# Optimization experiments

Measured on AMD Instinct MI355X. Metric: run time of the kernel, lower is better.

Reference implementation:

```python
import jax, jax.numpy as jnp
import numpy as np

B, S, D = 128, 50, 128
NUM_NODE = 40000
SAMPLE = 12
HOP = 2
ALPHA = 0.2  # leaky-relu slope (opt.alpha)


def _leaky(x, slope=ALPHA):
    return jnp.where(x >= 0, x, slope * x)


def setup_inputs() -> dict:
    key = jax.random.key(0)
    ks = jax.random.split(key, 12)
    stdv = 1.0 / float(np.sqrt(D))
    inputs = jax.random.randint(ks[0], (B, S), 0, NUM_NODE)
    adj = jax.random.randint(ks[1], (B, S, S), 0, 5)
    mask_item = jax.random.randint(ks[2], (B, S), 0, 2).at[:, 0].set(1)
    item = jax.random.randint(ks[3], (B, S), 0, NUM_NODE)
    adj_all = jax.random.randint(ks[4], (NUM_NODE, SAMPLE), 0, NUM_NODE)
    num_weight = jax.random.uniform(ks[5], (NUM_NODE, SAMPLE), dtype=jnp.float32)
    embedding = jax.random.uniform(ks[6], (NUM_NODE, D), minval=-stdv, maxval=stdv, dtype=jnp.float32)
    a_local = jax.random.uniform(ks[7], (4, D), minval=-stdv, maxval=stdv, dtype=jnp.float32)
    agg_w1 = jax.random.uniform(ks[8], (HOP, D + 1, D), minval=-stdv, maxval=stdv, dtype=jnp.float32)
    agg_w2 = jax.random.uniform(ks[9], (HOP, D, 1), minval=-stdv, maxval=stdv, dtype=jnp.float32)
    agg_w3 = jax.random.uniform(ks[10], (HOP, 2 * D, D), minval=-stdv, maxval=stdv, dtype=jnp.float32)
    return dict(inputs=inputs, adj=adj, mask_item=mask_item, item=item,
                adj_all=adj_all, num_weight=num_weight, embedding=embedding,
                a_local=a_local, agg_w1=agg_w1, agg_w2=agg_w2, agg_w3=agg_w3)


def _local_agg(h, adj, a_local):
    # e_k[b,i,j] = leakyrelu(sum_d h[b,i,d]*h[b,j,d]*a_k[d]); never materialize [B,N,N,D]
    e = _leaky(jnp.einsum('bid,bjd,kd->kbij', h, h, a_local))  # [4,B,S,S]
    alpha = jnp.full(e.shape[1:], -9e15, dtype=h.dtype)
    for k in range(4):
        alpha = jnp.where(adj == k + 1, e[k], alpha)
    alpha = jax.nn.softmax(alpha, axis=-1)
    return alpha @ h


def _global_agg(w1, w2, w3, self_v, neigh_v, neigh_w, extra):
    # self_v [B,L,D]; neigh_v [B,L,SAMPLE,D]; neigh_w [B,L,SAMPLE]; extra [B,L,D]
    feat = jnp.concatenate([extra[:, :, None, :] * neigh_v, neigh_w[..., None]], axis=-1)  # [B,L,SAMPLE,D+1]
    a = _leaky(feat @ w1, 0.2)                              # [B,L,SAMPLE,D]
    a = jax.nn.softmax((a @ w2)[..., 0], axis=-1)[..., None]  # [B,L,SAMPLE,1]
    neigh = jnp.sum(a * neigh_v, axis=-2)                   # [B,L,D]
    out = jnp.concatenate([self_v, neigh], axis=-1) @ w3    # [B,L,D]
    return jax.nn.relu(out)


def _forward(inputs, adj, mask_item, item, adj_all, num_weight, embedding,
             a_local, agg_w1, agg_w2, agg_w3):
    h = embedding[inputs]                          # [B,S,D]
    h_local = _local_agg(h, adj, a_local)
    # multi-hop neighbor sampling (index_select into adj_all / num)
    item_neighbors = [inputs]
    weight_neighbors = []
    support = S
    for _ in range(HOP):
        last = item_neighbors[-1].reshape(-1)
        support *= SAMPLE
        item_neighbors.append(adj_all[last].reshape(B, support))
        weight_neighbors.append(num_weight[last].reshape(B, support))
    entity = [embedding[idx] for idx in item_neighbors]
    mask_f = mask_item.astype(h.dtype)
    item_emb = embedding[item] * mask_f[..., None]
    session = (jnp.sum(item_emb, 1) / jnp.sum(mask_f, -1, keepdims=True))[:, None, :]  # [B,1,D]
    for n_hop in range(HOP):
        nxt = []
        for hop in range(HOP - n_hop):
            self_v = entity[hop]
            L = self_v.shape[1]
            neigh_v = entity[hop + 1].reshape(B, L, SAMPLE, D)
            neigh_w = weight_neighbors[hop].reshape(B, L, SAMPLE)
            extra = jnp.broadcast_to(session, (B, L, D))
            nxt.append(_global_agg(agg_w1[n_hop], agg_w2[n_hop], agg_w3[n_hop],
                                   self_v, neigh_v, neigh_w, extra))
        entity = nxt
    h_global = entity[0].reshape(B, S, D)
    # dropout_local / dropout_global are identity in eval mode
    return h_local + h_global


def reference(inputs, adj, mask_item, item, adj_all, num_weight, embedding,
              a_local, agg_w1, agg_w2, agg_w3):
    return _forward(inputs, adj, mask_item, item, adj_all, num_weight, embedding,
                    a_local, agg_w1, agg_w2, agg_w3)
```

## Files before the change

kernel.cpp:

```cpp
#include <hip/hip_runtime.h>
#include <math.h>

#define BATCH 128
#define S 50
#define D 128
#define SAMPLE 12

typedef __attribute__((ext_vector_type(8))) short short8v;
typedef __attribute__((ext_vector_type(4))) float f32x4;
typedef unsigned short u16;

__device__ __forceinline__ float leakyf(float x) { return x >= 0.f ? x : 0.2f * x; }
__device__ __forceinline__ u16 f2bf(float f) {
    union { float f; unsigned u; } v; v.f = f;
    unsigned u = v.u;
    return (u16)((u + 0x7FFFu + ((u >> 16) & 1u)) >> 16);
}
__device__ __forceinline__ float bf2f(u16 h) {
    union { float f; unsigned u; } v; v.u = ((unsigned)h) << 16; return v.f;
}

__global__ __launch_bounds__(256) void setup1_kernel(
    const int* __restrict__ item, const int* __restrict__ mask,
    const int* __restrict__ inputs, const int* __restrict__ adj_all,
    const float* __restrict__ num_weight, const float* __restrict__ emb,
    float* __restrict__ session, int* __restrict__ n1, float* __restrict__ nw0)
{
    const int bx = blockIdx.x, t = threadIdx.x;
    if (bx < BATCH) {
        if (t < 128) {
            float num = 0.f, den = 0.f;
            for (int s = 0; s < S; ++s) {
                float m = (float)mask[bx * S + s];
                num += m * emb[item[bx * S + s] * D + t];
                den += m;
            }
            session[bx * D + t] = num / den;
        }
    } else {
        int idx = (bx - BATCH) * 256 + t;
        if (idx < BATCH * 600) {
            int b = idx / 600, j = idx % 600;
            int node = inputs[b * S + j / SAMPLE];
            n1[idx]  = adj_all[node * SAMPLE + j % SAMPLE];
            nw0[idx] = num_weight[node * SAMPLE + j % SAMPLE];
        }
    }
}

__global__ __launch_bounds__(256) void prep2_kernel(
    const float* __restrict__ emb, const float* __restrict__ w1,
    const float* __restrict__ w3, const float* __restrict__ session,
    const int* __restrict__ adj_all, const float* __restrict__ num_weight,
    const int* __restrict__ n1,
    u16* __restrict__ emb_bf, u16* __restrict__ sw1, u16* __restrict__ w3t,
    int* __restrict__ n2p, int* __restrict__ n1p, float* __restrict__ nw1)
{
    const int bx = blockIdx.x, t = threadIdx.x;
    if (bx < 2500) {
        int idx = bx * 256 + t;
        const float4* src = reinterpret_cast<const float4*>(emb) + (size_t)idx * 2;
        float4 a = src[0], c = src[1];
        u16 o[8] = {f2bf(a.x), f2bf(a.y), f2bf(a.z), f2bf(a.w),
                    f2bf(c.x), f2bf(c.y), f2bf(c.z), f2bf(c.w)};
        *reinterpret_cast<uint4*>(emb_bf + (size_t)idx * 8) = *reinterpret_cast<uint4*>(o);
    } else if (bx < 2756) {
        int id = bx - 2500, hop = id >> 7, b = id & 127;
        const float* w1s = w1 + hop * 129 * 128;
        const float* se = session + b * 128;
        int n = t >> 1, kh = (t & 1) * 64;
        u16* dst = sw1 + (((size_t)(hop * 128 + b) * 128 + n) * 128) + kh;
        for (int kq = 0; kq < 64; kq += 8) {
            u16 o[8];
            #pragma unroll
            for (int e = 0; e < 8; ++e) { int k = kh + kq + e; o[e] = f2bf(w1s[k * 128 + n] * se[k]); }
            *reinterpret_cast<uint4*>(dst + kq) = *reinterpret_cast<uint4*>(o);
        }
    } else if (bx < 2788) {
        int j = (bx - 2756) * 256 + t;
        int hop = j >> 12, r = j & 4095, n = r >> 5, k0 = (r & 31) * 8;
        const float* w3s = w3 + hop * 256 * 128;
        u16 o[8];
        #pragma unroll
        for (int e = 0; e < 8; ++e) o[e] = f2bf(w3s[(k0 + e) * 128 + n]);
        *reinterpret_cast<uint4*>(w3t + ((size_t)hop * 128 + n) * 256 + k0) = *reinterpret_cast<uint4*>(o);
    } else if (bx < 6388) {
        int idx = (bx - 2788) * 256 + t;
        if (idx < BATCH * 7200) {
            int b = idx / 7200, r = idx % 7200;
            int lblk = r / 96, q = r % 96;
            int i = q >> 4, c = q & 15;
            int gm = lblk * 96 + (c >> 2) * 24 + i * 4 + (c & 3);
            int node = n1[b * 600 + gm / SAMPLE];
            int s = gm % SAMPLE;
            n2p[idx] = adj_all[node * SAMPLE + s] << 8;
            nw1[b * 7200 + gm] = num_weight[node * SAMPLE + s];
        }
    } else {
        int idx = (bx - 6388) * 256 + t;
        if (idx < BATCH * 672) {
            int b = idx / 672, r = idx % 672;
            int lblk = r / 96, q = r % 96;
            int i = q >> 4, c = q & 15;
            int gm = lblk * 96 + (c >> 2) * 24 + i * 4 + (c & 3);
            int jc = (gm < 600) ? gm : 0;
            n1p[idx] = n1[b * 600 + jc] << 8;
        }
    }
}

template <int PATH>
__global__ __launch_bounds__(256, 4) void main_kernel(
    const int* __restrict__ inputs, const int* __restrict__ adj,
    const u16* __restrict__ emb_bf, const float* __restrict__ a_local,
    const int* __restrict__ n1, const int* __restrict__ n2p,
    const int* __restrict__ n1p,
    const float* __restrict__ nw0, const float* __restrict__ nw1,
    const u16* __restrict__ sw1, const float* __restrict__ w1,
    const float* __restrict__ w2, const u16* __restrict__ w3t,
    const u16* __restrict__ in0, const u16* __restrict__ in1,
    u16* __restrict__ o0, u16* __restrict__ o1, float* __restrict__ outf)
{
    __shared__ __align__(16) char smem[30976];
    const int b = blockIdx.y;
    const int t = threadIdx.x;
    const int bx = blockIdx.x;

    if (PATH == 0 && bx == 0) {
        u16*   ht    = (u16*)smem;
        float* alpha = (float*)(smem + 13312);
        u16*   alb   = (u16*)(smem + 23520);

        for (int idx = t; idx < S * D; idx += 256) {
            int i = idx >> 7, d = idx & 127;
            ht[d * 52 + i] = emb_bf[(size_t)inputs[b * S + i] * D + d];
        }
        for (int idx = t; idx < 512; idx += 256) alb[idx] = f2bf(a_local[idx]);
        __syncthreads();

        for (int p = t; p < S * S; p += 256) {
            int i = p / S, j = p % S;
            int a = adj[b * S * S + p];
            float v = -9e15f;
            if (a >= 1 && a <= 4) {
                const u16* ak = alb + (a - 1) * D;
                float dot = 0.f;
                #pragma unroll 4
                for (int d = 0; d < D; ++d)
                    dot += bf2f(ht[d * 52 + i]) * bf2f(ht[d * 52 + j]) * bf2f(ak[d]);
                v = leakyf(dot);
            }
            alpha[i * 51 + j] = v;
        }
        __syncthreads();

        if (t < S) {
            float m = -INFINITY;
            for (int j = 0; j < S; ++j) m = fmaxf(m, alpha[t * 51 + j]);
            float ssum = 0.f;
            for (int j = 0; j < S; ++j) { float e = __expf(alpha[t * 51 + j] - m); alpha[t * 51 + j] = e; ssum += e; }
            float inv = 1.f / ssum;
            for (int j = 0; j < S; ++j) alpha[t * 51 + j] *= inv;
        }
        __syncthreads();

        for (int idx = t; idx < S * D; idx += 256) {
            int i = idx >> 7, d = idx & 127;
            float acc = 0.f;
            #pragma unroll 5
            for (int j = 0; j < S; ++j) acc += alpha[i * 51 + j] * bf2f(ht[d * 52 + j]);
            outf[(size_t)b * S * D + idx] = acc;
        }
        return;
    }

    int mode, lblk, L, Lm, hop;
    const u16 *nsrc, *ssrc;
    const int* ptab; const float* nwTab;
    u16* outb;
    if (PATH == 2)    { mode = 2; lblk = bx;     L = 50;  Lm = 600;  hop = 1; nsrc = in1;    ssrc = in0;    ptab = nullptr;                   nwTab = nw0; outb = nullptr; }
    else if (bx >= 8) { mode = 1; lblk = bx - 8; L = 600; Lm = 7200; hop = 0; nsrc = emb_bf; ssrc = emb_bf; ptab = n2p + (b * 75 + lblk) * 96; nwTab = nw1; outb = o1; }
    else              { mode = 0; lblk = bx - 1; L = 50;  Lm = 600;  hop = 0; nsrc = emb_bf; ssrc = emb_bf; ptab = n1p + (b * 7 + lblk) * 96;  nwTab = nw0; outb = o0; }
    const int l0 = lblk * 8;

    u16*   nvL     = (u16*)smem;
    u16*   selfL   = (u16*)(smem + 24576);
    float* score_w = (float*)(smem + 28672);
    float* nwgtL   = (float*)(smem + 30208);
    float* alphL   = (float*)(smem + 30592);

    const u16*   sw1b   = sw1 + (size_t)(hop * 128 + b) * 16384;
    const float* w1last = w1 + hop * 129 * 128 + 128 * 128;
    const float* w2h    = w2 + hop * 128;
    const u16*   w3th   = w3t + hop * 32768;

    const int lane = t & 63, wv = t >> 6, cn = lane & 15, cg = lane >> 4;
    const int nc0 = (2 * wv) * 16 + cn, nc1 = (2 * wv + 1) * 16 + cn;
    const int c = t & 15;
    const int chunk = t >> 4;

    #pragma unroll
    for (int i = 0; i < 6; ++i) {
        int off;
        if (PATH == 2) {
            int gm = l0 * 12 + (c >> 2) * 24 + i * 4 + (c & 3);
            if (gm > 599) gm = 599;
            off = (b * 600 + gm) << 8;
        } else {
            off = ptab[i * 16 + c];
        }
        uint4 v = *reinterpret_cast<const uint4*>((const char*)nsrc + (unsigned)off + chunk * 16);
        *reinterpret_cast<uint4*>(nvL + (i * 256 + t) * 8) = v;
    }
    {
        int l = 2 * (c >> 2) + ((c >> 1) & 1);
        int lg = l0 + l; if (lg >= L) lg = 0;
        int srow;
        if (PATH == 2)      srow = b * 50 + lg;
        else if (mode == 1) srow = n1[b * 600 + lg];
        else                srow = inputs[b * S + lg];
        uint4 v = *reinterpret_cast<const uint4*>(ssrc + (size_t)srow * 128 + chunk * 8);
        *reinterpret_cast<uint4*>(selfL + t * 8) = v;
    }
    if (t < 96) {
        int gm = l0 * 12 + t;
        nwgtL[t] = (gm < Lm) ? nwTab[b * Lm + gm] : 0.f;
    }
    __syncthreads();

    f32x4 acc[6][2];
    #pragma unroll
    for (int mt = 0; mt < 6; ++mt) {
        acc[mt][0] = (f32x4){0.f, 0.f, 0.f, 0.f};
        acc[mt][1] = (f32x4){0.f, 0.f, 0.f, 0.f};
    }
    #pragma unroll
    for (int kk = 0; kk < 4; ++kk) {
        int kb = kk * 32 + cg * 8;
        short8v b0 = *reinterpret_cast<const short8v*>(sw1b + nc0 * 128 + kb);
        short8v b1 = *reinterpret_cast<const short8v*>(sw1b + nc1 * 128 + kb);
        #pragma unroll
        for (int mt = 0; mt < 6; ++mt) {
            short8v a = *reinterpret_cast<const short8v*>(nvL + ((mt * 4 + kk) * 64 + lane) * 8);
            acc[mt][0] = __builtin_amdgcn_mfma_f32_16x16x32_bf16(a, b0, acc[mt][0], 0, 0, 0);
            acc[mt][1] = __builtin_amdgcn_mfma_f32_16x16x32_bf16(a, b1, acc[mt][1], 0, 0, 0);
        }
    }
    {
        float w2v0 = w2h[nc0], w2v1 = w2h[nc1];
        float w1l0 = w1last[nc0], w1l1 = w1last[nc1];
        #pragma unroll
        for (int mt = 0; mt < 6; ++mt) {
            #pragma unroll
            for (int r = 0; r < 4; ++r) {
                int m = cg * 24 + mt * 4 + r;
                float nw = nwgtL[m];
                float v = leakyf(acc[mt][0][r] + nw * w1l0) * w2v0 +
                          leakyf(acc[mt][1][r] + nw * w1l1) * w2v1;
                v += __shfl_xor(v, 1); v += __shfl_xor(v, 2);
                v += __shfl_xor(v, 4); v += __shfl_xor(v, 8);
                if (cn == 0) score_w[m * 4 + wv] = v;
            }
        }
    }
    __syncthreads();

    {
        float alph[24];
        const f32x4* sw4 = reinterpret_cast<const f32x4*>(score_w);
        float mx0 = -1e30f, mx1 = -1e30f;
        #pragma unroll
        for (int q = 0; q < 24; ++q) {
            f32x4 s4 = sw4[cg * 24 + q];
            float s = (s4[0] + s4[1]) + (s4[2] + s4[3]);
            alph[q] = s;
            if (q < 12) mx0 = fmaxf(mx0, s); else mx1 = fmaxf(mx1, s);
        }
        float sm0 = 0.f, sm1 = 0.f;
        #pragma unroll
        for (int q = 0; q < 12; ++q) { alph[q] = __expf(alph[q] - mx0); sm0 += alph[q]; }
        #pragma unroll
        for (int q = 12; q < 24; ++q) { alph[q] = __expf(alph[q] - mx1); sm1 += alph[q]; }
        float i0 = 1.f / sm0, i1 = 1.f / sm1;
        if (cn == 0) {
            #pragma unroll
            for (int q = 0; q < 12; ++q)  alphL[cg * 24 + q] = alph[q] * i0;
            #pragma unroll
            for (int q = 12; q < 24; ++q) alphL[cg * 24 + q] = alph[q] * i1;
        }
    }

    volatile const float* alphV = alphL;
    #pragma unroll
    for (int j = 0; j < 2; ++j) {
        int nc = (2 * wv + j) * 16 + cn;
        f32x4 Y[6]; f32x4 Ys = (f32x4){0.f, 0.f, 0.f, 0.f};
        #pragma unroll
        for (int mt = 0; mt < 6; ++mt) Y[mt] = (f32x4){0.f, 0.f, 0.f, 0.f};
        #pragma unroll
        for (int kk = 0; kk < 4; ++kk) {
            int kb = kk * 32 + cg * 8;
            short8v bw = *reinterpret_cast<const short8v*>(w3th + nc * 256 + 128 + kb);
            short8v bs = *reinterpret_cast<const short8v*>(w3th + nc * 256 + kb);
            short8v aS = *reinterpret_cast<const short8v*>(selfL + (kk * 64 + lane) * 8);
            Ys = __builtin_amdgcn_mfma_f32_16x16x32_bf16(aS, bs, Ys, 0, 0, 0);
            #pragma unroll
            for (int mt = 0; mt < 6; ++mt) {
                short8v a = *reinterpret_cast<const short8v*>(nvL + ((mt * 4 + kk) * 64 + lane) * 8);
                Y[mt] = __builtin_amdgcn_mfma_f32_16x16x32_bf16(a, bw, Y[mt], 0, 0, 0);
            }
        }
        float P0 = 0.f, P1 = 0.f;
        #pragma unroll
        for (int q = 0; q < 12; ++q) P0 += alphV[cg * 24 + q] * Y[q >> 2][q & 3];
        #pragma unroll
        for (int q = 12; q < 24; ++q) P1 += alphV[cg * 24 + q] * Y[q >> 2][q & 3];
        float v0 = fmaxf(P0 + Ys[0], 0.f);
        float v1 = fmaxf(P1 + Ys[2], 0.f);
        int lg0 = l0 + cg * 2, lg1 = lg0 + 1;
        if (PATH == 2) {
            if (lg0 < L) { float* p = outf + ((size_t)b * 50 + lg0) * 128 + nc; *p += v0; }
            if (lg1 < L) { float* p = outf + ((size_t)b * 50 + lg1) * 128 + nc; *p += v1; }
        } else {
            if (lg0 < L) outb[((size_t)b * L + lg0) * 128 + nc] = f2bf(v0);
            if (lg1 < L) outb[((size_t)b * L + lg1) * 128 + nc] = f2bf(v1);
        }
    }
}

extern "C" void kernel_launch(void* const* d_in, const int* in_sizes, int n_in,
                              void* d_out, int out_size, void* d_ws, size_t ws_size,
                              hipStream_t stream)
{
    const int*   inputs     = (const int*)d_in[0];
    const int*   adj        = (const int*)d_in[1];
    const int*   mask_item  = (const int*)d_in[2];
    const int*   item       = (const int*)d_in[3];
    const int*   adj_all    = (const int*)d_in[4];
    const float* num_weight = (const float*)d_in[5];
    const float* embedding  = (const float*)d_in[6];
    const float* a_local    = (const float*)d_in[7];
    const float* agg_w1     = (const float*)d_in[8];
    const float* agg_w2     = (const float*)d_in[9];
    const float* agg_w3     = (const float*)d_in[10];
    float* out = (float*)d_out;

    char* w = (char*)d_ws;
    float* ws_session = (float*)(w);
    int*   ws_n1      = (int*)(w + 65536);
    float* ws_nw0     = (float*)(w + 372736);
    float* ws_nw1     = (float*)(w + 679936);
    int*   ws_n2p     = (int*)(w + 4366336);
    int*   ws_n1p     = (int*)(w + 8052736);
    u16*   ws_emb     = (u16*)(w + 8396800);
    u16*   ws_sw1     = (u16*)(w + 18636800);
    u16*   ws_w3t     = (u16*)(w + 27025408);
    u16*   ws_out0    = (u16*)(w + 27156480);
    u16*   ws_out1    = (u16*)(w + 28794880);

    setup1_kernel<<<dim3(BATCH + 300), 256, 0, stream>>>(
        item, mask_item, inputs, adj_all, num_weight, embedding,
        ws_session, ws_n1, ws_nw0);
    prep2_kernel<<<dim3(6724), 256, 0, stream>>>(
        embedding, agg_w1, agg_w3, ws_session, adj_all, num_weight, ws_n1,
        ws_emb, ws_sw1, ws_w3t, ws_n2p, ws_n1p, ws_nw1);

    main_kernel<0><<<dim3(83, BATCH), 256, 0, stream>>>(
        inputs, adj, ws_emb, a_local, ws_n1, ws_n2p, ws_n1p, ws_nw0, ws_nw1,
        ws_sw1, agg_w1, agg_w2, ws_w3t,
        nullptr, nullptr, ws_out0, ws_out1, out);

    main_kernel<2><<<dim3(7, BATCH), 256, 0, stream>>>(
        inputs, adj, ws_emb, a_local, ws_n1, ws_n2p, ws_n1p, ws_nw0, ws_nw1,
        ws_sw1, agg_w1, agg_w2, ws_w3t,
        ws_out0, ws_out1, nullptr, nullptr, out);
}
```

Before: 348.6 us.

## Aggregate neighbors before W3 GEMM and swizzle LDS tile layout

Reorders the math so the softmax-weighted sum of neighbor embeddings is formed first (in LDS, converted to bf16), then a single concatenated [self|neigh] x W3 MFMA GEMM runs over K=256. This replaces the earlier scheme of multiplying every neighbor sample by W3 and reducing afterwards, which cuts the second-stage MFMA work by roughly the sample count. The neighbor tile is also XOR-swizzled in LDS so the aggregation reads avoid bank conflicts. The cost is an extra LDS pass, a barrier and a little more shared memory, and the aggregated vector is rounded to bf16 before the GEMM.

```diff
diff --git a/kernel.cpp b/kernel.cpp
--- a/kernel.cpp
+++ b/kernel.cpp
@@ -109,6 +109,8 @@
     }
 }
 
+__device__ __forceinline__ int swz(int cg, int kk) { return ((kk & 1) << 2) | cg; }
+
 template <int PATH>
 __global__ __launch_bounds__(256, 4) void main_kernel(
     const int* __restrict__ inputs, const int* __restrict__ adj,
@@ -121,7 +123,7 @@
     const u16* __restrict__ in0, const u16* __restrict__ in1,
     u16* __restrict__ o0, u16* __restrict__ o1, float* __restrict__ outf)
 {
-    __shared__ __align__(16) char smem[30976];
+    __shared__ __align__(16) char smem[35072];
     const int b = blockIdx.y;
     const int t = threadIdx.x;
     const int bx = blockIdx.x;
@@ -184,10 +186,10 @@
     const int l0 = lblk * 8;
 
     u16*   nvL     = (u16*)smem;
-    u16*   selfL   = (u16*)(smem + 24576);
-    float* score_w = (float*)(smem + 28672);
-    float* nwgtL   = (float*)(smem + 30208);
-    float* alphL   = (float*)(smem + 30592);
+    u16*   A2      = (u16*)(smem + 24576);
+    float* score_w = (float*)(smem + 32768);
+    float* nwgtL   = (float*)(smem + 34304);
+    float* alphL   = (float*)(smem + 34688);
 
     const u16*   sw1b   = sw1 + (size_t)(hop * 128 + b) * 16384;
     const float* w1last = w1 + hop * 129 * 128 + 128 * 128;
@@ -196,31 +198,41 @@
 
     const int lane = t & 63, wv = t >> 6, cn = lane & 15, cg = lane >> 4;
     const int nc0 = (2 * wv) * 16 + cn, nc1 = (2 * wv + 1) * 16 + cn;
-    const int c = t & 15;
+    const int cS = t & 15;
     const int chunk = t >> 4;
 
-    #pragma unroll
-    for (int i = 0; i < 6; ++i) {
-        int off;
-        if (PATH == 2) {
-            int gm = l0 * 12 + (c >> 2) * 24 + i * 4 + (c & 3);
-            if (gm > 599) gm = 599;
-            off = (b * 600 + gm) << 8;
-        } else {
-            off = ptab[i * 16 + c];
-        }
-        uint4 v = *reinterpret_cast<const uint4*>((const char*)nsrc + (unsigned)off + chunk * 16);
-        *reinterpret_cast<uint4*>(nvL + (i * 256 + t) * 8) = v;
-    }
     {
-        int l = 2 * (c >> 2) + ((c >> 1) & 1);
-        int lg = l0 + l; if (lg >= L) lg = 0;
-        int srow;
-        if (PATH == 2)      srow = b * 50 + lg;
-        else if (mode == 1) srow = n1[b * 600 + lg];
-        else                srow = inputs[b * S + lg];
-        uint4 v = *reinterpret_cast<const uint4*>(ssrc + (size_t)srow * 128 + chunk * 8);
-        *reinterpret_cast<uint4*>(selfL + t * 8) = v;
+        int kkS = t >> 6, cgS = (t >> 4) & 3;
+        int cn2 = cS ^ swz(cgS, kkS);
+        #pragma unroll
+        for (int i = 0; i < 6; ++i) {
+            int off;
+            if (PATH == 2) {
+                int gm = l0 * 12 + (cn2 >> 2) * 24 + i * 4 + (cn2 & 3);
+                if (gm > 599) gm = 599;
+                off = (b * 600 + gm) << 8;
+            } else {
+                off = ptab[i * 16 + cn2];
+            }
+            uint4 v = *reinterpret_cast<const uint4*>((const char*)nsrc + (unsigned)off + chunk * 16);
+            *reinterpret_cast<uint4*>(nvL + (i * 256 + t) * 8) = v;
+        }
+    }
+    {
+        uint4 v = make_uint4(0, 0, 0, 0);
+        if (cS < 8) {
+            int lg = l0 + cS; if (lg >= L) lg = 0;
+            int srow;
+            if (PATH == 2)      srow = b * 50 + lg;
+            else if (mode == 1) srow = n1[b * 600 + lg];
+            else                srow = inputs[b * S + lg];
+            v = *reinterpret_cast<const uint4*>(ssrc + (size_t)srow * 128 + chunk * 8);
+        }
+        *reinterpret_cast<uint4*>(A2 + t * 8) = v;
+    }
+    if (t < 128) {
+        int slot = (4 + (t >> 5)) * 64 + ((t >> 3) & 3) * 16 + 8 + (t & 7);
+        *reinterpret_cast<uint4*>(A2 + slot * 8) = make_uint4(0, 0, 0, 0);
     }
     if (t < 96) {
         int gm = l0 * 12 + t;
@@ -237,11 +249,12 @@
     #pragma unroll
     for (int kk = 0; kk < 4; ++kk) {
         int kb = kk * 32 + cg * 8;
+        int lslot = cg * 16 + (cn ^ swz(cg, kk));
         short8v b0 = *reinterpret_cast<const short8v*>(sw1b + nc0 * 128 + kb);
         short8v b1 = *reinterpret_cast<const short8v*>(sw1b + nc1 * 128 + kb);
         #pragma unroll
         for (int mt = 0; mt < 6; ++mt) {
-            short8v a = *reinterpret_cast<const short8v*>(nvL + ((mt * 4 + kk) * 64 + lane) * 8);
+            short8v a = *reinterpret_cast<const short8v*>(nvL + ((mt * 4 + kk) * 64 + lslot) * 8);
             acc[mt][0] = __builtin_amdgcn_mfma_f32_16x16x32_bf16(a, b0, acc[mt][0], 0, 0, 0);
             acc[mt][1] = __builtin_amdgcn_mfma_f32_16x16x32_bf16(a, b1, acc[mt][1], 0, 0, 0);
         }
@@ -284,46 +297,52 @@
         float i0 = 1.f / sm0, i1 = 1.f / sm1;
         if (cn == 0) {
             #pragma unroll
-            for (int q = 0; q < 12; ++q)  alphL[cg * 24 + q] = alph[q] * i0;
-            #pragma unroll
-            for (int q = 12; q < 24; ++q) alphL[cg * 24 + q] = alph[q] * i1;
-        }
-    }
-
-    volatile const float* alphV = alphL;
+            for (int q = 0; q < 12; ++q)  alphL[(cg * 2) * 12 + q] = alph[q] * i0;
+            #pragma unroll
+            for (int q = 12; q < 24; ++q) alphL[(cg * 2 + 1) * 12 + (q - 12)] = alph[q] * i1;
+        }
+    }
+
+    #pragma unroll 1
+    for (int i = 0; i < 4; ++i) {
+        int idx = i * 256 + t;
+        int l = idx >> 7, d = idx & 127;
+        int kkd = d >> 5, cgd = (d >> 3) & 3, el = d & 7;
+        int cnb = (l >> 1) * 4;
+        int mtb = (l & 1) * 3;
+        int fd = swz(cgd, kkd);
+        float a = 0.f;
+        #pragma unroll
+        for (int s = 0; s < 12; ++s) {
+            int slot = ((mtb + (s >> 2)) * 4 + kkd) * 64 + cgd * 16 + ((cnb + (s & 3)) ^ fd);
+            a += alphL[l * 12 + s] * bf2f(nvL[slot * 8 + el]);
+        }
+        int slot2 = (4 + kkd) * 64 + cgd * 16 + l;
+        A2[slot2 * 8 + el] = f2bf(a);
+    }
+    __syncthreads();
+
     #pragma unroll
     for (int j = 0; j < 2; ++j) {
         int nc = (2 * wv + j) * 16 + cn;
-        f32x4 Y[6]; f32x4 Ys = (f32x4){0.f, 0.f, 0.f, 0.f};
-        #pragma unroll
-        for (int mt = 0; mt < 6; ++mt) Y[mt] = (f32x4){0.f, 0.f, 0.f, 0.f};
-        #pragma unroll
-        for (int kk = 0; kk < 4; ++kk) {
-            int kb = kk * 32 + cg * 8;
-            short8v bw = *reinterpret_cast<const short8v*>(w3th + nc * 256 + 128 + kb);
-            short8v bs = *reinterpret_cast<const short8v*>(w3th + nc * 256 + kb);
-            short8v aS = *reinterpret_cast<const short8v*>(selfL + (kk * 64 + lane) * 8);
-            Ys = __builtin_amdgcn_mfma_f32_16x16x32_bf16(aS, bs, Ys, 0, 0, 0);
-            #pragma unroll
-            for (int mt = 0; mt < 6; ++mt) {
-                short8v a = *reinterpret_cast<const short8v*>(nvL + ((mt * 4 + kk) * 64 + lane) * 8);
-                Y[mt] = __builtin_amdgcn_mfma_f32_16x16x32_bf16(a, bw, Y[mt], 0, 0, 0);
-            }
-        }
-        float P0 = 0.f, P1 = 0.f;
-        #pragma unroll
-        for (int q = 0; q < 12; ++q) P0 += alphV[cg * 24 + q] * Y[q >> 2][q & 3];
-        #pragma unroll
-        for (int q = 12; q < 24; ++q) P1 += alphV[cg * 24 + q] * Y[q >> 2][q & 3];
-        float v0 = fmaxf(P0 + Ys[0], 0.f);
-        float v1 = fmaxf(P1 + Ys[2], 0.f);
-        int lg0 = l0 + cg * 2, lg1 = lg0 + 1;
-        if (PATH == 2) {
-            if (lg0 < L) { float* p = outf + ((size_t)b * 50 + lg0) * 128 + nc; *p += v0; }
-            if (lg1 < L) { float* p = outf + ((size_t)b * 50 + lg1) * 128 + nc; *p += v1; }
-        } else {
-            if (lg0 < L) outb[((size_t)b * L + lg0) * 128 + nc] = f2bf(v0);
-            if (lg1 < L) outb[((size_t)b * L + lg1) * 128 + nc] = f2bf(v1);
+        f32x4 acc2 = (f32x4){0.f, 0.f, 0.f, 0.f};
+        #pragma unroll
+        for (int kk2 = 0; kk2 < 8; ++kk2) {
+            short8v a2 = *reinterpret_cast<const short8v*>(A2 + (kk2 * 64 + lane) * 8);
+            short8v bb = *reinterpret_cast<const short8v*>(w3th + nc * 256 + kk2 * 32 + cg * 8);
+            acc2 = __builtin_amdgcn_mfma_f32_16x16x32_bf16(a2, bb, acc2, 0, 0, 0);
+        }
+        if (cg < 2) {
+            #pragma unroll
+            for (int r = 0; r < 4; ++r) {
+                int l = cg * 4 + r;
+                int lg = l0 + l;
+                float v = fmaxf(acc2[r], 0.f);
+                if (lg < L) {
+                    if (PATH == 2) { float* p = outf + ((size_t)b * 50 + lg) * 128 + nc; *p += v; }
+                    else           outb[((size_t)b * L + lg) * 128 + nc] = f2bf(v);
+                }
+            }
         }
     }
 }
```

New measurement: 356.6 us. 1.02x slower.
